# Kernel optimization log

Hardware: AMD Instinct MI355X
Metric: run time of the kernel (lower is better)

Reference implementation:

```python
import jax, jax.numpy as jnp
import numpy as np

HO, WO = 64, 64
SHARPNESS = 150.0


def _stereographic_grid(ho, wo):
    # Matches create_normal_grid(..., 'stereographic'); torch.meshgrid 'ij':
    # v varies over rows (ho), u over cols (wo).
    v, u = np.meshgrid(np.arange(ho), np.arange(wo), indexing='ij')
    p = 4.0 * ((u + 0.5) / wo - 0.5)
    q = -4.0 * ((v + 0.5) / ho - 0.5)
    d = 1.0 + p ** 2 + q ** 2
    z = -(-1.0 + p ** 2 + q ** 2) / d
    m = (z > 0.0).astype(np.float32)
    x = 2.0 * p / d * m
    y = 2.0 * q / d * m
    z = z * m
    return np.stack([x, y, z], axis=-1).reshape(-1, 3).astype(np.float32)  # [ho*wo,3]


_GRID = _stereographic_grid(HO, WO)
_IDX = np.nonzero(np.any(_GRID != 0, axis=-1))[0]  # static valid-query indices [N]
_QN = _GRID[_IDX]  # [N,3]


def setup_inputs() -> dict:
    key = jax.random.key(0)
    k1, k2, k3 = jax.random.split(key, 3)
    bs, c, h, w = 2, 64, 192, 192
    in_fea_map = jax.random.normal(k1, (bs, c, h, w), dtype=jnp.float32)
    nrm = jax.random.normal(k2, (bs, 3, h, w), dtype=jnp.float32)
    in_normal_map = nrm / (jnp.linalg.norm(nrm, axis=1, keepdims=True) + 1e-8)
    in_mask_map = (jax.random.uniform(k3, (bs, 1, h, w)) > 0.2).astype(jnp.float32)
    log_query_norm = jnp.full((1,), np.log(SHARPNESS), dtype=jnp.float32)
    return {"in_fea_map": in_fea_map, "in_normal_map": in_normal_map,
            "in_mask_map": in_mask_map, "log_query_norm": log_query_norm}


def reference(in_fea_map, in_normal_map, in_mask_map, log_query_norm):
    bs, c, h, w = in_fea_map.shape
    hw = h * w
    qn = jnp.asarray(_QN, dtype=in_fea_map.dtype)  # [N,3] static valid queries
    vals = in_fea_map.reshape(bs, c, hw).transpose(0, 2, 1)       # [bs,HW,c]
    key_n = in_normal_map.reshape(bs, 3, hw)                       # [bs,3,HW]
    cos = jnp.einsum('nd,bdm->bnm', qn, key_n)                     # [bs,N,HW]
    dps = cos / np.float32(np.sqrt(3.0))
    dps = dps - jnp.max(dps, axis=-1, keepdims=True)
    w_ = jnp.exp(jnp.exp(log_query_norm) * dps)                    # dropout in eval = identity
    w_ = w_ * in_mask_map.reshape(bs, 1, hw)
    weights = w_ / (jnp.sum(w_, axis=-1, keepdims=True) + 1e-9)    # [bs,N,HW]
    mapped = weights @ vals                                        # [bs,N,c]
    mapped = jnp.concatenate([jnp.broadcast_to(qn, (bs,) + qn.shape), mapped], axis=-1)
    # variance map over last 3 feature channels
    mean = mapped[..., -3:]
    sq_mean = weights @ (vals[..., -3:] ** 2)
    var = jnp.sum(sq_mean - mean ** 2, axis=-1, keepdims=True)
    mapped = jnp.concatenate([var, mapped], axis=-1)
    # cosine map
    rm_cos = jnp.sum(weights * cos, axis=-1, keepdims=True)
    mapped = jnp.concatenate([rm_cos, mapped], axis=-1)            # [bs,N,c+5]
    C = mapped.shape[-1]
    out = jnp.zeros((bs, HO * WO, C), mapped.dtype).at[:, _IDX, :].set(mapped)
    return out.transpose(0, 2, 1).reshape(bs, C, HO, WO)
```

## Files before the change

kernel.cpp:

```cpp
#include <hip/hip_runtime.h>
#include <cstdint>
#include <cstddef>

#define HW 36864
#define QT 64

constexpr bool is_valid_px(int v, int u) {
  int a = 2 * u - 63, b = 2 * v - 63;
  return a * a + b * b < 1024;
}
constexpr int count_valid() {
  int n = 0;
  for (int v = 0; v < 64; ++v)
    for (int u = 0; u < 64; ++u)
      if (is_valid_px(v, u)) ++n;
  return n;
}
constexpr int NV  = count_valid();
constexpr int NQT = (NV + QT - 1) / QT;
constexpr int NQP = NQT * QT;
constexpr int PLANE = 2 * NQP * 69;

struct QTab { short idx[NQP]; };
constexpr QTab make_qtab() {
  QTab t{};
  int n = 0;
  for (int p = 0; p < 4096; ++p) {
    int v = p >> 6, u = p & 63;
    if (is_valid_px(v, u)) { t.idx[n] = (short)p; ++n; }
  }
  for (int i = n; i < NQP; ++i) t.idx[i] = -1;
  return t;
}
__constant__ QTab g_qtab = make_qtab();

typedef short short8 __attribute__((ext_vector_type(8)));
typedef float f32x4  __attribute__((ext_vector_type(4)));

__device__ __forceinline__ unsigned short f2b(float f) {
  unsigned int u = __float_as_uint(f);
  u += 0x7FFFu + ((u >> 16) & 1u);
  return (unsigned short)(u >> 16);
}
__device__ __forceinline__ ushort4 f2b4(float4 v) {
  ushort4 r; r.x = f2b(v.x); r.y = f2b(v.y); r.z = f2b(v.z); r.w = f2b(v.w);
  return r;
}
__device__ __forceinline__ void pix2qn(int pix, float& x, float& y, float& z) {
  x = 0.f; y = 0.f; z = 0.f;
  if (pix >= 0) {
    int v = pix >> 6, u = pix & 63;
    float p = (float)(2 * u - 63) * (1.0f / 32.0f);
    float q = -(float)(2 * v - 63) * (1.0f / 32.0f);
    float d = 1.0f + p * p + q * q;
    x = 2.0f * p / d; y = 2.0f * q / d; z = (1.0f - p * p - q * q) / d;
  }
}


template<int KSC>
__global__ __launch_bounds__(256) void partial_kernel(
    const float* __restrict__ fea,
    const float* __restrict__ nrm,
    const float* __restrict__ msk,
    const float* __restrict__ lqn,
    float* __restrict__ part)
{
  constexpr int SLICE  = HW / KSC;
  constexpr int NCHUNK = SLICE / 64;

  __shared__ __align__(16) unsigned short v_s[2][80][72];
  __shared__ __align__(16) float nrm4_s[2][64][4];
  __shared__ float ex_s[64][9];

  const int bx  = blockIdx.x;
  const int cls = bx & 7;
  const int r0  = bx >> 3;
  const int qt  = r0 % NQT;
  const int sh  = r0 / NQT;
  const int s   = sh * 8 + cls;
  const int b   = s / KSC;
  const int ks  = s % KSC;

  const int t    = threadIdx.x;
  const int wv   = t >> 6;
  const int l    = t & 63;
  const int lq   = l >> 4;
  const int mrow = l & 15;

  const float Cc = __expf(lqn[0]) * 0.57735026919f;

  float qx, qy, qz;
  pix2qn(g_qtab.idx[qt * QT + 16 * wv + mrow], qx, qy, qz);

  if (t < 160) {
    int row = 70 + (t >> 4);
    int p4  = (t & 15) * 4;
    unsigned short c = (row == 70) ? (unsigned short)0x3F80 : (unsigned short)0;
    ushort4 cv; cv.x = c; cv.y = c; cv.z = c; cv.w = c;
    *(ushort4*)&v_s[0][row][p4] = cv;
    *(ushort4*)&v_s[1][row][p4] = cv;
  }

  const size_t base_f = (size_t)b * 64 * HW;
  const size_t base_n = (size_t)b * 3 * HW;
  const size_t base_m = (size_t)b * HW;

  const int chb = t >> 4;
  const int px4 = (t & 15) * 4;
  const int arr = t >> 6;
  const int pxp = 32 * (l >> 5) + 4 * (l & 7) + ((l >> 3) & 3);

  f32x4 acc[5];
  #pragma unroll
  for (int nt = 0; nt < 5; ++nt) acc[nt] = (f32x4)(0.0f);

  float4 pf[4];
  float pn = 0.f, pm = 0.f;

  auto load_chunk = [&](int ck) {
    int m0 = ks * SLICE + ck * 64;
    #pragma unroll
    for (int i = 0; i < 4; ++i)
      pf[i] = *(const float4*)(fea + base_f + (size_t)(chb + 16 * i) * HW + (size_t)(m0 + px4));
    if (arr < 3) pn = nrm[base_n + (size_t)arr * HW + (size_t)(m0 + l)];
    else         pm = msk[base_m + (size_t)(m0 + l)];
  };
  auto store_chunk = [&](int buf) {
    #pragma unroll
    for (int i = 0; i < 4; ++i) {
      int ch = chb + 16 * i;
      float4 fv = pf[i];
      *(ushort4*)&v_s[buf][ch][px4] = f2b4(fv);
      if (ch >= 61) {
        float4 sq = make_float4(fv.x * fv.x, fv.y * fv.y, fv.z * fv.z, fv.w * fv.w);
        *(ushort4*)&v_s[buf][ch + 3][px4] = f2b4(sq);
      }
    }
    if (arr < 3) {
      v_s[buf][67 + arr][l] = f2b(pn);
      nrm4_s[buf][pxp][arr] = Cc * pn;
    } else {
      nrm4_s[buf][pxp][3] = -Cc + (pm > 0.5f ? 0.f : -2000.f);
    }
  };

  load_chunk(0);
  store_chunk(0);
  __syncthreads();

  for (int ck = 0; ck < NCHUNK; ++ck) {
    const int buf = ck & 1;
    if (ck + 1 < NCHUNK) load_chunk(ck + 1);

    #pragma unroll
    for (int kk = 0; kk < 64; kk += 32) {
      short8 a;
      #pragma unroll
      for (int j = 0; j < 8; ++j) {
        const float4 nv = *(const float4*)&nrm4_s[buf][kk + 4 * j + lq][0];
        float tt = fmaf(qx, nv.x, fmaf(qy, nv.y, fmaf(qz, nv.z, nv.w)));
        a[j] = (short)f2b(__expf(tt));
      }
      #pragma unroll
      for (int nt = 0; nt < 5; ++nt) {
        short8 bb = *(const short8*)&v_s[buf][16 * nt + mrow][kk + 8 * lq];
        acc[nt] = __builtin_amdgcn_mfma_f32_16x16x32_bf16(a, bb, acc[nt], 0, 0, 0);
      }
    }

    if (ck + 1 < NCHUNK) {
      store_chunk(buf ^ 1);
      __syncthreads();
    }
  }

  const size_t pbase = (size_t)ks * PLANE + ((size_t)b * NQP + (size_t)(qt * QT)) * 69;
  #pragma unroll
  for (int nt = 0; nt < 4; ++nt) {
    #pragma unroll
    for (int rr = 0; rr < 4; ++rr) {
      int qloc = 16 * wv + 4 * lq + rr;
      part[pbase + (size_t)qloc * 69 + (size_t)(16 * nt + mrow)] = acc[nt][rr];
    }
  }
  if (mrow < 7) {
    #pragma unroll
    for (int rr = 0; rr < 4; ++rr)
      ex_s[16 * wv + 4 * lq + rr][mrow] = acc[4][rr];
  }
  __syncthreads();
  if (t < 64) {
    float gx, gy, gz;
    pix2qn(g_qtab.idx[qt * QT + t], gx, gy, gz);
    float swc = gx * ex_s[t][3] + gy * ex_s[t][4] + gz * ex_s[t][5];
    size_t o = pbase + (size_t)t * 69;
    part[o + 64] = ex_s[t][0];
    part[o + 65] = ex_s[t][1];
    part[o + 66] = ex_s[t][2];
    part[o + 67] = swc;
    part[o + 68] = ex_s[t][6];
  }
}

__global__ __launch_bounds__(128) void reduce_scatter_kernel(
    const float* __restrict__ part,
    float* __restrict__ out,
    int ksc)
{
  const int bq = blockIdx.x;
  const int q  = bq % NQP;
  const int b  = bq / NQP;
  const int t  = threadIdx.x;

  const int pix = g_qtab.idx[q];
  if (pix < 0) return;

  __shared__ float pv[69];
  if (t < 69) {
    float s = 0.f;
    for (int k = 0; k < ksc; ++k)
      s += part[(size_t)k * PLANE + (size_t)bq * 69 + (size_t)t];
    pv[t] = s;
  }
  __syncthreads();

  const float inv = 1.0f / (pv[68] + 1e-9f);
  float val = 0.f;
  if (t == 0) {
    val = pv[67] * inv;
  } else if (t == 1) {
    #pragma unroll
    for (int i = 0; i < 3; ++i) {
      float m  = pv[61 + i] * inv;
      float sq = pv[64 + i] * inv;
      val += sq - m * m;
    }
  } else if (t < 5) {
    float gx, gy, gz;
    pix2qn(pix, gx, gy, gz);
    val = (t == 2) ? gx : (t == 3) ? gy : gz;
  } else if (t < 69) {
    val = pv[t - 5] * inv;
  }
  if (t < 69) out[(size_t)(b * 69 + t) * 4096 + pix] = val;
}

extern "C" void kernel_launch(void* const* d_in, const int* in_sizes, int n_in,
                              void* d_out, int out_size, void* d_ws, size_t ws_size,
                              hipStream_t stream) {
  const float* fea = (const float*)d_in[0];
  const float* nrm = (const float*)d_in[1];
  const float* msk = (const float*)d_in[2];
  const float* lqn = (const float*)d_in[3];
  float* part = (float*)d_ws;
  float* out  = (float*)d_out;

  hipMemsetAsync(d_out, 0, (size_t)out_size * sizeof(float), stream);

  const size_t need32 = (size_t)PLANE * 32 * sizeof(float);
  if (ws_size >= need32) {
    partial_kernel<32><<<dim3(2 * 32 * NQT), 256, 0, stream>>>(fea, nrm, msk, lqn, part);
    reduce_scatter_kernel<<<dim3(2 * NQP), 128, 0, stream>>>(part, out, 32);
  } else {
    partial_kernel<16><<<dim3(2 * 16 * NQT), 256, 0, stream>>>(fea, nrm, msk, lqn, part);
    reduce_scatter_kernel<<<dim3(2 * NQP), 128, 0, stream>>>(part, out, 16);
  }
}
```

Measured before the change: 123.2 us.

## Replace split-K partial planes with atomic accumulation and larger K split

Raises the key split from 32 to 64 slices and has each block atomically add its partial sums into one shared accumulator, instead of writing separate per-slice planes that a later kernel sums. A new normalize kernel then reads one accumulator per query tile and writes the scattered output, and the per-query cosine dot with the query direction moves out of the partial kernel into it. The bf16 conversion now uses paired hardware conversion. This removes the large partial-buffer write and re-read traffic at the cost of atomic contention, an extra memset, and a non-deterministic summation order.

```diff
diff --git a/kernel.cpp b/kernel.cpp
--- a/kernel.cpp
+++ b/kernel.cpp
@@ -1,9 +1,14 @@
 #include <hip/hip_runtime.h>
+#include <hip/hip_bf16.h>
 #include <cstdint>
 #include <cstddef>
 
 #define HW 36864
 #define QT 64
+#define KSC 64
+#define NCH 72
+constexpr int SLICE  = HW / KSC;
+constexpr int NCHUNK = SLICE / 64;
 
 constexpr bool is_valid_px(int v, int u) {
   int a = 2 * u - 63, b = 2 * v - 63;
@@ -19,7 +24,6 @@
 constexpr int NV  = count_valid();
 constexpr int NQT = (NV + QT - 1) / QT;
 constexpr int NQP = NQT * QT;
-constexpr int PLANE = 2 * NQP * 69;
 
 struct QTab { short idx[NQP]; };
 constexpr QTab make_qtab() {
@@ -42,8 +46,14 @@
   u += 0x7FFFu + ((u >> 16) & 1u);
   return (unsigned short)(u >> 16);
 }
+__device__ __forceinline__ ushort2 f2b2(float a, float b) {
+  __hip_bfloat162 h = __float22bfloat162_rn(make_float2(a, b));
+  return *(ushort2*)&h;
+}
 __device__ __forceinline__ ushort4 f2b4(float4 v) {
-  ushort4 r; r.x = f2b(v.x); r.y = f2b(v.y); r.z = f2b(v.z); r.w = f2b(v.w);
+  ushort4 r;
+  *(ushort2*)&r.x = f2b2(v.x, v.y);
+  *(ushort2*)&r.z = f2b2(v.z, v.w);
   return r;
 }
 __device__ __forceinline__ void pix2qn(int pix, float& x, float& y, float& z) {
@@ -58,20 +68,15 @@
 }
 
 
-template<int KSC>
 __global__ __launch_bounds__(256) void partial_kernel(
     const float* __restrict__ fea,
     const float* __restrict__ nrm,
     const float* __restrict__ msk,
     const float* __restrict__ lqn,
-    float* __restrict__ part)
+    float* __restrict__ accum)
 {
-  constexpr int SLICE  = HW / KSC;
-  constexpr int NCHUNK = SLICE / 64;
-
   __shared__ __align__(16) unsigned short v_s[2][80][72];
   __shared__ __align__(16) float nrm4_s[2][64][4];
-  __shared__ float ex_s[64][9];
 
   const int bx  = blockIdx.x;
   const int cls = bx & 7;
@@ -79,8 +84,8 @@
   const int qt  = r0 % NQT;
   const int sh  = r0 / NQT;
   const int s   = sh * 8 + cls;
-  const int b   = s / KSC;
-  const int ks  = s % KSC;
+  const int b   = s >> 6;
+  const int ks  = s & 63;
 
   const int t    = threadIdx.x;
   const int wv   = t >> 6;
@@ -155,12 +160,19 @@
 
     #pragma unroll
     for (int kk = 0; kk < 64; kk += 32) {
-      short8 a;
+      float e[8];
       #pragma unroll
       for (int j = 0; j < 8; ++j) {
         const float4 nv = *(const float4*)&nrm4_s[buf][kk + 4 * j + lq][0];
         float tt = fmaf(qx, nv.x, fmaf(qy, nv.y, fmaf(qz, nv.z, nv.w)));
-        a[j] = (short)f2b(__expf(tt));
+        e[j] = __expf(tt);
+      }
+      short8 a;
+      #pragma unroll
+      for (int p = 0; p < 4; ++p) {
+        ushort2 pr = f2b2(e[2 * p], e[2 * p + 1]);
+        a[2 * p]     = (short)pr.x;
+        a[2 * p + 1] = (short)pr.y;
       }
       #pragma unroll
       for (int nt = 0; nt < 5; ++nt) {
@@ -175,75 +187,71 @@
     }
   }
 
-  const size_t pbase = (size_t)ks * PLANE + ((size_t)b * NQP + (size_t)(qt * QT)) * 69;
+  const size_t abase = ((size_t)b * NQP + (size_t)(qt * QT)) * NCH;
   #pragma unroll
   for (int nt = 0; nt < 4; ++nt) {
     #pragma unroll
     for (int rr = 0; rr < 4; ++rr) {
       int qloc = 16 * wv + 4 * lq + rr;
-      part[pbase + (size_t)qloc * 69 + (size_t)(16 * nt + mrow)] = acc[nt][rr];
+      atomicAdd(&accum[abase + (size_t)qloc * NCH + (size_t)(16 * nt + mrow)], acc[nt][rr]);
     }
   }
   if (mrow < 7) {
     #pragma unroll
-    for (int rr = 0; rr < 4; ++rr)
-      ex_s[16 * wv + 4 * lq + rr][mrow] = acc[4][rr];
-  }
+    for (int rr = 0; rr < 4; ++rr) {
+      int qloc = 16 * wv + 4 * lq + rr;
+      atomicAdd(&accum[abase + (size_t)qloc * NCH + (size_t)(64 + mrow)], acc[4][rr]);
+    }
+  }
+}
+
+__global__ __launch_bounds__(256) void normalize_kernel(
+    const float* __restrict__ accum,
+    float* __restrict__ out)
+{
+  __shared__ float a_s[64][NCH];
+
+  const int blk = blockIdx.x;
+  const int qt  = blk % NQT;
+  const int b   = blk / NQT;
+  const int t   = threadIdx.x;
+
+  const float* src = accum + ((size_t)b * NQP + (size_t)(qt * QT)) * NCH;
+  for (int i = t; i < 64 * NCH; i += 256) ((float*)a_s)[i] = src[i];
   __syncthreads();
-  if (t < 64) {
-    float gx, gy, gz;
-    pix2qn(g_qtab.idx[qt * QT + t], gx, gy, gz);
-    float swc = gx * ex_s[t][3] + gy * ex_s[t][4] + gz * ex_s[t][5];
-    size_t o = pbase + (size_t)t * 69;
-    part[o + 64] = ex_s[t][0];
-    part[o + 65] = ex_s[t][1];
-    part[o + 66] = ex_s[t][2];
-    part[o + 67] = swc;
-    part[o + 68] = ex_s[t][6];
-  }
-}
-
-__global__ __launch_bounds__(128) void reduce_scatter_kernel(
-    const float* __restrict__ part,
-    float* __restrict__ out,
-    int ksc)
-{
-  const int bq = blockIdx.x;
-  const int q  = bq % NQP;
-  const int b  = bq / NQP;
-  const int t  = threadIdx.x;
-
-  const int pix = g_qtab.idx[q];
+
+  const int q   = t & 63;
+  const int grp = t >> 6;
+  const int pix = g_qtab.idx[qt * QT + q];
   if (pix < 0) return;
 
-  __shared__ float pv[69];
-  if (t < 69) {
-    float s = 0.f;
-    for (int k = 0; k < ksc; ++k)
-      s += part[(size_t)k * PLANE + (size_t)bq * 69 + (size_t)t];
-    pv[t] = s;
-  }
-  __syncthreads();
-
-  const float inv = 1.0f / (pv[68] + 1e-9f);
-  float val = 0.f;
-  if (t == 0) {
-    val = pv[67] * inv;
-  } else if (t == 1) {
+  const float* A = a_s[q];
+  const float inv = 1.0f / (A[70] + 1e-9f);
+  float gx, gy, gz;
+  pix2qn(pix, gx, gy, gz);
+  float* ob = out + (size_t)b * 69 * 4096 + pix;
+
+  if (grp == 0) {
+    float rm = (gx * A[67] + gy * A[68] + gz * A[69]) * inv;
+    float var = 0.f;
     #pragma unroll
     for (int i = 0; i < 3; ++i) {
-      float m  = pv[61 + i] * inv;
-      float sq = pv[64 + i] * inv;
-      val += sq - m * m;
-    }
-  } else if (t < 5) {
-    float gx, gy, gz;
-    pix2qn(pix, gx, gy, gz);
-    val = (t == 2) ? gx : (t == 3) ? gy : gz;
-  } else if (t < 69) {
-    val = pv[t - 5] * inv;
-  }
-  if (t < 69) out[(size_t)(b * 69 + t) * 4096 + pix] = val;
+      float m  = A[61 + i] * inv;
+      float sq = A[64 + i] * inv;
+      var += sq - m * m;
+    }
+    ob[0 * 4096] = rm;
+    ob[1 * 4096] = var;
+    ob[2 * 4096] = gx;
+    ob[3 * 4096] = gy;
+    ob[4 * 4096] = gz;
+    #pragma unroll
+    for (int c = 0; c < 13; ++c) ob[(size_t)(5 + c) * 4096] = A[c] * inv;
+  } else {
+    int c0 = 13 + (grp - 1) * 17;
+    #pragma unroll
+    for (int c = 0; c < 17; ++c) ob[(size_t)(5 + c0 + c) * 4096] = A[c0 + c] * inv;
+  }
 }
 
 extern "C" void kernel_launch(void* const* d_in, const int* in_sizes, int n_in,
@@ -253,17 +261,11 @@
   const float* nrm = (const float*)d_in[1];
   const float* msk = (const float*)d_in[2];
   const float* lqn = (const float*)d_in[3];
-  float* part = (float*)d_ws;
-  float* out  = (float*)d_out;
-
+  float* accum = (float*)d_ws;
+  float* out   = (float*)d_out;
+
+  hipMemsetAsync(accum, 0, (size_t)2 * NQP * NCH * sizeof(float), stream);
   hipMemsetAsync(d_out, 0, (size_t)out_size * sizeof(float), stream);
-
-  const size_t need32 = (size_t)PLANE * 32 * sizeof(float);
-  if (ws_size >= need32) {
-    partial_kernel<32><<<dim3(2 * 32 * NQT), 256, 0, stream>>>(fea, nrm, msk, lqn, part);
-    reduce_scatter_kernel<<<dim3(2 * NQP), 128, 0, stream>>>(part, out, 32);
-  } else {
-    partial_kernel<16><<<dim3(2 * 16 * NQT), 256, 0, stream>>>(fea, nrm, msk, lqn, part);
-    reduce_scatter_kernel<<<dim3(2 * NQP), 128, 0, stream>>>(part, out, 16);
-  }
-}
+  partial_kernel<<<dim3(2 * KSC * NQT), 256, 0, stream>>>(fea, nrm, msk, lqn, accum);
+  normalize_kernel<<<dim3(2 * NQT), 256, 0, stream>>>(accum, out);
+}
```

After: 129.6 us. +5.2%, slower.

## Fuse output zeroing into finalize kernel and use packed bf16 conversion

Applied to the files above, without the earlier changes.

Removes the separate memset of the output and folds zero-filling of invalid pixels into a new finalize kernel. That kernel reduces 16 queries per block with coalesced partial reads through shared memory, replacing the old one-query-per-block reduction. It also switches the float-to-bf16 rounding to the packed two-at-a-time intrinsic in the hot MFMA loop and in staging. The result is one fewer launch and less scattered reduction traffic, at the cost of a fixed 256-block grid whose tail blocks stride over the whole output.

```diff
diff --git a/kernel.cpp b/kernel.cpp
--- a/kernel.cpp
+++ b/kernel.cpp
@@ -1,9 +1,11 @@
 #include <hip/hip_runtime.h>
+#include <hip/hip_bf16.h>
 #include <cstdint>
 #include <cstddef>
 
 #define HW 36864
 #define QT 64
+#define NCHA 69
 
 constexpr bool is_valid_px(int v, int u) {
   int a = 2 * u - 63, b = 2 * v - 63;
@@ -19,15 +21,19 @@
 constexpr int NV  = count_valid();
 constexpr int NQT = (NV + QT - 1) / QT;
 constexpr int NQP = NQT * QT;
-constexpr int PLANE = 2 * NQP * 69;
-
-struct QTab { short idx[NQP]; };
+constexpr int PLANE = 2 * NQP * NCHA;
+
+struct QTab {
+  short idx[NQP];
+  short rank[4096];
+};
 constexpr QTab make_qtab() {
   QTab t{};
   int n = 0;
   for (int p = 0; p < 4096; ++p) {
     int v = p >> 6, u = p & 63;
-    if (is_valid_px(v, u)) { t.idx[n] = (short)p; ++n; }
+    if (is_valid_px(v, u)) { t.idx[n] = (short)p; t.rank[p] = (short)n; ++n; }
+    else t.rank[p] = -1;
   }
   for (int i = n; i < NQP; ++i) t.idx[i] = -1;
   return t;
@@ -42,8 +48,14 @@
   u += 0x7FFFu + ((u >> 16) & 1u);
   return (unsigned short)(u >> 16);
 }
+__device__ __forceinline__ ushort2 f2b2(float a, float b) {
+  __hip_bfloat162 h = __float22bfloat162_rn(make_float2(a, b));
+  return *(ushort2*)&h;
+}
 __device__ __forceinline__ ushort4 f2b4(float4 v) {
-  ushort4 r; r.x = f2b(v.x); r.y = f2b(v.y); r.z = f2b(v.z); r.w = f2b(v.w);
+  ushort4 r;
+  *(ushort2*)&r.x = f2b2(v.x, v.y);
+  *(ushort2*)&r.z = f2b2(v.z, v.w);
   return r;
 }
 __device__ __forceinline__ void pix2qn(int pix, float& x, float& y, float& z) {
@@ -155,12 +167,19 @@
 
     #pragma unroll
     for (int kk = 0; kk < 64; kk += 32) {
-      short8 a;
+      float e[8];
       #pragma unroll
       for (int j = 0; j < 8; ++j) {
         const float4 nv = *(const float4*)&nrm4_s[buf][kk + 4 * j + lq][0];
         float tt = fmaf(qx, nv.x, fmaf(qy, nv.y, fmaf(qz, nv.z, nv.w)));
-        a[j] = (short)f2b(__expf(tt));
+        e[j] = __expf(tt);
+      }
+      short8 a;
+      #pragma unroll
+      for (int p = 0; p < 4; ++p) {
+        ushort2 pr = f2b2(e[2 * p], e[2 * p + 1]);
+        a[2 * p]     = (short)pr.x;
+        a[2 * p + 1] = (short)pr.y;
       }
       #pragma unroll
       for (int nt = 0; nt < 5; ++nt) {
@@ -175,13 +194,13 @@
     }
   }
 
-  const size_t pbase = (size_t)ks * PLANE + ((size_t)b * NQP + (size_t)(qt * QT)) * 69;
+  const size_t pbase = (size_t)ks * PLANE + ((size_t)b * NQP + (size_t)(qt * QT)) * NCHA;
   #pragma unroll
   for (int nt = 0; nt < 4; ++nt) {
     #pragma unroll
     for (int rr = 0; rr < 4; ++rr) {
       int qloc = 16 * wv + 4 * lq + rr;
-      part[pbase + (size_t)qloc * 69 + (size_t)(16 * nt + mrow)] = acc[nt][rr];
+      part[pbase + (size_t)qloc * NCHA + (size_t)(16 * nt + mrow)] = acc[nt][rr];
     }
   }
   if (mrow < 7) {
@@ -194,7 +213,7 @@
     float gx, gy, gz;
     pix2qn(g_qtab.idx[qt * QT + t], gx, gy, gz);
     float swc = gx * ex_s[t][3] + gy * ex_s[t][4] + gz * ex_s[t][5];
-    size_t o = pbase + (size_t)t * 69;
+    size_t o = pbase + (size_t)t * NCHA;
     part[o + 64] = ex_s[t][0];
     part[o + 65] = ex_s[t][1];
     part[o + 66] = ex_s[t][2];
@@ -203,47 +222,69 @@
   }
 }
 
-__global__ __launch_bounds__(128) void reduce_scatter_kernel(
+#define NFIN (2 * NQT * 4)
+#define NTAIL 256
+
+__global__ __launch_bounds__(256) void finalize_kernel(
     const float* __restrict__ part,
     float* __restrict__ out,
     int ksc)
 {
-  const int bq = blockIdx.x;
-  const int q  = bq % NQP;
-  const int b  = bq / NQP;
-  const int t  = threadIdx.x;
-
-  const int pix = g_qtab.idx[q];
-  if (pix < 0) return;
-
-  __shared__ float pv[69];
-  if (t < 69) {
-    float s = 0.f;
-    for (int k = 0; k < ksc; ++k)
-      s += part[(size_t)k * PLANE + (size_t)bq * 69 + (size_t)t];
-    pv[t] = s;
-  }
-  __syncthreads();
-
-  const float inv = 1.0f / (pv[68] + 1e-9f);
-  float val = 0.f;
-  if (t == 0) {
-    val = pv[67] * inv;
-  } else if (t == 1) {
-    #pragma unroll
-    for (int i = 0; i < 3; ++i) {
-      float m  = pv[61 + i] * inv;
-      float sq = pv[64 + i] * inv;
-      val += sq - m * m;
-    }
-  } else if (t < 5) {
-    float gx, gy, gz;
-    pix2qn(pix, gx, gy, gz);
-    val = (t == 2) ? gx : (t == 3) ? gy : gz;
-  } else if (t < 69) {
-    val = pv[t - 5] * inv;
-  }
-  if (t < 69) out[(size_t)(b * 69 + t) * 4096 + pix] = val;
+  const int blk = blockIdx.x;
+  const int t   = threadIdx.x;
+
+  if (blk < NFIN) {
+    __shared__ float sm[16][NCHA];
+    const int b   = blk / (NQT * 4);
+    const int rem = blk % (NQT * 4);
+    const int qt  = rem >> 2;
+    const int qr  = rem & 3;
+    const int q0  = qt * QT + qr * 16;
+
+    const size_t colbase = ((size_t)b * NQP + (size_t)q0) * NCHA;
+    for (int i = t; i < 16 * NCHA; i += 256) {
+      float sv = 0.f;
+      const size_t off = colbase + (size_t)i;
+      #pragma unroll 8
+      for (int k = 0; k < ksc; ++k) sv += part[(size_t)k * PLANE + off];
+      sm[0][i] = sv;
+    }
+    __syncthreads();
+
+    for (int i = t; i < 16 * NCHA; i += 256) {
+      const int ql = i / NCHA;
+      const int oc = i % NCHA;
+      const int pix = g_qtab.idx[q0 + ql];
+      if (pix < 0) continue;
+      const float* A = sm[ql];
+      const float inv = 1.0f / (A[68] + 1e-9f);
+      float gx, gy, gz;
+      pix2qn(pix, gx, gy, gz);
+      float val;
+      if (oc == 0)      val = A[67] * inv;
+      else if (oc == 1) {
+        val = 0.f;
+        #pragma unroll
+        for (int j = 0; j < 3; ++j) {
+          float m  = A[61 + j] * inv;
+          float sq = A[64 + j] * inv;
+          val += sq - m * m;
+        }
+      }
+      else if (oc == 2) val = gx;
+      else if (oc == 3) val = gy;
+      else if (oc == 4) val = gz;
+      else              val = A[oc - 5] * inv;
+      out[((size_t)b * NCHA + (size_t)oc) * 4096 + pix] = val;
+    }
+  } else {
+    const int start = (blk - NFIN) * 256 + t;
+    const int strd  = (NTAIL - NFIN) * 256;
+    const int TOT   = 2 * NCHA * 4096;
+    for (int i = start; i < TOT; i += strd) {
+      if (g_qtab.rank[i & 4095] < 0) out[i] = 0.0f;
+    }
+  }
 }
 
 extern "C" void kernel_launch(void* const* d_in, const int* in_sizes, int n_in,
@@ -256,14 +297,12 @@
   float* part = (float*)d_ws;
   float* out  = (float*)d_out;
 
-  hipMemsetAsync(d_out, 0, (size_t)out_size * sizeof(float), stream);
-
   const size_t need32 = (size_t)PLANE * 32 * sizeof(float);
   if (ws_size >= need32) {
     partial_kernel<32><<<dim3(2 * 32 * NQT), 256, 0, stream>>>(fea, nrm, msk, lqn, part);
-    reduce_scatter_kernel<<<dim3(2 * NQP), 128, 0, stream>>>(part, out, 32);
+    finalize_kernel<<<dim3(NTAIL), 256, 0, stream>>>(part, out, 32);
   } else {
     partial_kernel<16><<<dim3(2 * 16 * NQT), 256, 0, stream>>>(fea, nrm, msk, lqn, part);
-    reduce_scatter_kernel<<<dim3(2 * NQP), 128, 0, stream>>>(part, out, 16);
-  }
-}
+    finalize_kernel<<<dim3(NTAIL), 256, 0, stream>>>(part, out, 16);
+  }
+}
```

Result: no change. 122.0 us (-0.9%).
